# Kernel tuning notes

Measured on AMD Instinct MI355X. Metric: run time of the kernel, lower is better.

Reference implementation:

```python
import jax, jax.numpy as jnp
import numpy as np

B, T, E = 32, 4096, 256
L = T // 2  # static clipped_length, enforced by construction in setup_inputs
THRESHOLD = 0.0


def setup_inputs() -> dict:
    key = jax.random.key(0)
    k1, k2, k3 = jax.random.split(key, 3)
    x = jax.random.normal(k1, (B, T, E), dtype=jnp.float32)
    # Force channel 0 (the padding channel) to be strictly negative for t < L
    # and strictly positive for t >= L, so every example keeps exactly the
    # first L timesteps and clipped_length == L deterministically.
    mag = jnp.abs(jax.random.normal(k2, (B, T), dtype=jnp.float32)) + 0.1
    sign = jnp.where(jnp.arange(T) < L, -1.0, 1.0)[None, :]
    x = x.at[:, :, 0].set(sign * mag)
    padding_amount = jax.random.normal(k3, (1,), dtype=jnp.float32)
    return {"x": x, "padding_amount": padding_amount, "clipped_length": L}


def reference(x, padding_amount, clipped_length):
    # x: [B, T, E]; channel 0 = padding scalar, channels 1: = signal
    Bsz, Tlen, Edim = x.shape
    Lc = clipped_length  # static python int
    pad = x[:, :, 0] * (1.0 + jnp.abs(padding_amount[0]))  # [B, T]
    sig = x[:, :, 1:]                                      # [B, T, E-1]
    # The original only scans the first clipped_length timesteps when compacting.
    keep = pad[:, :Lc] < THRESHOLD                         # [B, L]
    # Stream compaction: exclusive running count gives destination slot.
    dest = jnp.cumsum(keep.astype(jnp.int32), axis=1) - 1  # [B, L]
    dest = jnp.where(keep, dest, Lc)                       # dropped -> dummy slot L
    vals = jnp.concatenate([pad[:, :Lc, None], sig[:, :Lc]], axis=-1)  # [B, L, E]
    # Base: channel 0 filled with threshold, rest zeros (matches original init).
    base = jnp.zeros((Bsz, Lc + 1, Edim), dtype=x.dtype).at[:, :, 0].set(THRESHOLD)
    bidx = jnp.arange(Bsz)[:, None]
    out = base.at[bidx, dest].set(vals)
    return out[:, :Lc]  # drop dummy slot -> [B, clipped_length, E]
```

## Files before the change

### kernel.cpp

```cpp
#include <hip/hip_runtime.h>
#include <hip/hip_bf16.h>

constexpr int B = 32;
constexpr int T = 4096;
constexpr int E = 256;
constexpr int L = T / 2;
constexpr int E4 = E / 4;

__global__ __launch_bounds__(256) void scan_kernel(
    const float* __restrict__ x,
    const float* __restrict__ pad_amt,
    int* __restrict__ srcmap,
    int* __restrict__ count)
{
    const int b   = blockIdx.x;
    const int tid = threadIdx.x;
    const float scale = 1.0f + fabsf(pad_amt[0]);

    int keep[8];
    int s = 0;
#pragma unroll
    for (int i = 0; i < 8; ++i) {
        const int t = tid * 8 + i;
        const float pad = x[(size_t)(b * T + t) * E] * scale;
        keep[i] = (pad < 0.0f) ? 1 : 0;
        s += keep[i];
    }

    const int lane = tid & 63;
    const int wave = tid >> 6;
    int inc = s;
#pragma unroll
    for (int off = 1; off < 64; off <<= 1) {
        int n = __shfl_up(inc, off, 64);
        if (lane >= off) inc += n;
    }

    __shared__ int wsum[4];
    if (lane == 63) wsum[wave] = inc;
    __syncthreads();

    int wbase = 0;
#pragma unroll
    for (int w = 0; w < 3; ++w)
        if (w < wave) wbase += wsum[w];

    const int excl = wbase + inc - s;

    int run = excl;
#pragma unroll
    for (int i = 0; i < 8; ++i) {
        if (keep[i]) {
            srcmap[b * L + run] = tid * 8 + i;
            ++run;
        }
    }

    if (tid == 0)
        count[b] = wsum[0] + wsum[1] + wsum[2] + wsum[3];
}

__global__ __launch_bounds__(256) void gather_kernel(
    const float* __restrict__ x,
    const float* __restrict__ pad_amt,
    const int* __restrict__ srcmap,
    const int* __restrict__ count,
    float* __restrict__ out)
{
    const int g   = blockIdx.x * 256 + threadIdx.x;
    const int row = g >> 6;
    const int d   = g & 63;
    const int b   = row >> 11;
    const int j   = row & (L - 1);

    float4 v;
    if (j < count[b]) {
        const int t = srcmap[row];
        const float4* src = reinterpret_cast<const float4*>(x)
                          + (size_t)(b * T + t) * E4;
        v = src[d];
        if (d == 0)
            v.x *= (1.0f + fabsf(pad_amt[0]));
    } else {
        v = make_float4(0.0f, 0.0f, 0.0f, 0.0f);
    }
    reinterpret_cast<float4*>(out)[g] = v;
}

extern "C" void kernel_launch(void* const* d_in, const int* in_sizes, int n_in,
                              void* d_out, int out_size, void* d_ws, size_t ws_size,
                              hipStream_t stream)
{
    const float* x       = reinterpret_cast<const float*>(d_in[0]);
    const float* pad_amt = reinterpret_cast<const float*>(d_in[1]);

    int* count  = reinterpret_cast<int*>(d_ws);
    int* srcmap = reinterpret_cast<int*>(d_ws) + 64;

    scan_kernel<<<B, 256, 0, stream>>>(x, pad_amt, srcmap, count);

    const int total_f4 = B * L * E4;
    gather_kernel<<<total_f4 / 256, 256, 0, stream>>>(x, pad_amt, srcmap, count,
                                                      reinterpret_cast<float*>(d_out));
}
```

Before: 204.3 us.

## Widen scan block, encode dropped rows as -1, give each gather thread four float4s

Result: no change. 203.5 us (-0.4%).

```diff
diff --git a/kernel.cpp b/kernel.cpp
--- a/kernel.cpp
+++ b/kernel.cpp
@@ -1,31 +1,26 @@
 #include <hip/hip_runtime.h>
 #include <hip/hip_bf16.h>
 
-constexpr int B = 32;
-constexpr int T = 4096;
-constexpr int E = 256;
-constexpr int L = T / 2;
+constexpr int B  = 32;
+constexpr int T  = 4096;
+constexpr int E  = 256;
+constexpr int L  = T / 2;
 constexpr int E4 = E / 4;
 
-__global__ __launch_bounds__(256) void scan_kernel(
+__global__ __launch_bounds__(1024) void scan_kernel(
     const float* __restrict__ x,
-    const float* __restrict__ pad_amt,
-    int* __restrict__ srcmap,
-    int* __restrict__ count)
+    int* __restrict__ srcmap)
 {
     const int b   = blockIdx.x;
     const int tid = threadIdx.x;
-    const float scale = 1.0f + fabsf(pad_amt[0]);
+    const int t0  = tid * 2;
 
-    int keep[8];
-    int s = 0;
-#pragma unroll
-    for (int i = 0; i < 8; ++i) {
-        const int t = tid * 8 + i;
-        const float pad = x[(size_t)(b * T + t) * E] * scale;
-        keep[i] = (pad < 0.0f) ? 1 : 0;
-        s += keep[i];
-    }
+    const size_t base = (size_t)b * T * E;
+    const float a0 = x[base + (size_t)t0 * E];
+    const float a1 = x[base + (size_t)(t0 + 1) * E];
+    const int k0 = (a0 < 0.0f) ? 1 : 0;
+    const int k1 = (a1 < 0.0f) ? 1 : 0;
+    const int s  = k0 + k1;
 
     const int lane = tid & 63;
     const int wave = tid >> 6;
@@ -36,55 +31,57 @@
         if (lane >= off) inc += n;
     }
 
-    __shared__ int wsum[4];
+    __shared__ int wsum[16];
     if (lane == 63) wsum[wave] = inc;
     __syncthreads();
 
-    int wbase = 0;
+    int wbase = 0, total = 0;
 #pragma unroll
-    for (int w = 0; w < 3; ++w)
-        if (w < wave) wbase += wsum[w];
+    for (int w = 0; w < 16; ++w) {
+        const int v = wsum[w];
+        if (w < wave) wbase += v;
+        total += v;
+    }
 
     const int excl = wbase + inc - s;
+    int* __restrict__ sm = srcmap + b * L;
+    if (k0) sm[excl]      = t0;
+    if (k1) sm[excl + k0] = t0 + 1;
 
-    int run = excl;
-#pragma unroll
-    for (int i = 0; i < 8; ++i) {
-        if (keep[i]) {
-            srcmap[b * L + run] = tid * 8 + i;
-            ++run;
-        }
-    }
-
-    if (tid == 0)
-        count[b] = wsum[0] + wsum[1] + wsum[2] + wsum[3];
+    for (int k = total + tid; k < L; k += 1024)
+        sm[k] = -1;
 }
 
 __global__ __launch_bounds__(256) void gather_kernel(
     const float* __restrict__ x,
     const float* __restrict__ pad_amt,
     const int* __restrict__ srcmap,
-    const int* __restrict__ count,
     float* __restrict__ out)
 {
-    const int g   = blockIdx.x * 256 + threadIdx.x;
-    const int row = g >> 6;
-    const int d   = g & 63;
-    const int b   = row >> 11;
-    const int j   = row & (L - 1);
+    const int r   = blockIdx.x * 16 + (threadIdx.x >> 4);
+    const int l16 = threadIdx.x & 15;
+    const int t   = srcmap[r];
+    const int b   = r >> 11;
 
-    float4 v;
-    if (j < count[b]) {
-        const int t = srcmap[row];
-        const float4* src = reinterpret_cast<const float4*>(x)
-                          + (size_t)(b * T + t) * E4;
-        v = src[d];
-        if (d == 0)
-            v.x *= (1.0f + fabsf(pad_amt[0]));
+    float4 v0, v1, v2, v3;
+    if (t >= 0) {
+        const float4* __restrict__ s =
+            reinterpret_cast<const float4*>(x) + ((size_t)(b * T) + t) * E4;
+        v0 = s[ 0 + l16];
+        v1 = s[16 + l16];
+        v2 = s[32 + l16];
+        v3 = s[48 + l16];
+        if (l16 == 0)
+            v0.x *= (1.0f + fabsf(pad_amt[0]));
     } else {
-        v = make_float4(0.0f, 0.0f, 0.0f, 0.0f);
+        v0 = v1 = v2 = v3 = make_float4(0.f, 0.f, 0.f, 0.f);
     }
-    reinterpret_cast<float4*>(out)[g] = v;
+
+    float4* __restrict__ o = reinterpret_cast<float4*>(out) + (size_t)r * E4;
+    o[ 0 + l16] = v0;
+    o[16 + l16] = v1;
+    o[32 + l16] = v2;
+    o[48 + l16] = v3;
 }
 
 extern "C" void kernel_launch(void* const* d_in, const int* in_sizes, int n_in,
@@ -94,12 +91,10 @@
     const float* x       = reinterpret_cast<const float*>(d_in[0]);
     const float* pad_amt = reinterpret_cast<const float*>(d_in[1]);
 
-    int* count  = reinterpret_cast<int*>(d_ws);
-    int* srcmap = reinterpret_cast<int*>(d_ws) + 64;
+    int* srcmap = reinterpret_cast<int*>(d_ws);
 
-    scan_kernel<<<B, 256, 0, stream>>>(x, pad_amt, srcmap, count);
+    scan_kernel<<<B, 1024, 0, stream>>>(x, srcmap);
 
-    const int total_f4 = B * L * E4;
-    gather_kernel<<<total_f4 / 256, 256, 0, stream>>>(x, pad_amt, srcmap, count,
-                                                      reinterpret_cast<float*>(d_out));
+    gather_kernel<<<(B * L) / 16, 256, 0, stream>>>(
+        x, pad_amt, srcmap, reinterpret_cast<float*>(d_out));
 }
```
